# Performance work log

Measured on AMD Instinct MI355X. Metric: run time of the kernel, lower is better.

The kernel has to match this reference:

```python
import jax, jax.numpy as jnp
import numpy as np

B, Q, CACHE, CROSS = 16, 16, 1024, 1024
D, H, DK, DFF = 1024, 16, 64, 4096
EPS = 1e-5


def _ln(x, g, b):
    mu = jnp.mean(x, axis=-1, keepdims=True)
    var = jnp.mean(jnp.square(x - mu), axis=-1, keepdims=True)
    return (x - mu) * jax.lax.rsqrt(var + EPS) * g + b


def _heads(t):  # [B, L, D] -> [B, H, L, DK]
    return t.reshape(t.shape[0], t.shape[1], H, DK).transpose(0, 2, 1, 3)


def _attn(q, k, v, mask):  # q:[B,H,Q,DK] k,v:[B,H,L,DK] mask:[B,Q,L] bool
    scores = jnp.einsum('bhqd,bhkd->bhqk', q, k) / np.sqrt(DK).astype(np.float32)
    scores = jnp.where(mask[:, None, :, :], scores, jnp.finfo(scores.dtype).min)
    p = jax.nn.softmax(scores, axis=-1)
    o = jnp.einsum('bhqk,bhkd->bhqd', p, v)
    return o.transpose(0, 2, 1, 3).reshape(q.shape[0], q.shape[2], D)


def setup_inputs() -> dict:
    key = jax.random.key(0)
    ks = jax.random.split(key, 24)
    s = 0.02
    inp = {
        'x': jax.random.normal(ks[0], (B, Q, D), jnp.float32),
        'self_k_cache': jax.random.normal(ks[1], (B, CACHE, D), jnp.float32),
        'self_v_cache': jax.random.normal(ks[2], (B, CACHE, D), jnp.float32),
        'cross_k': jax.random.normal(ks[3], (B, CROSS, D), jnp.float32),
        'cross_v': jax.random.normal(ks[4], (B, CROSS, D), jnp.float32),
        'self_attn_mask': jnp.ones((B, Q, CACHE), jnp.bool_),
        'cross_attn_mask': jnp.ones((B, Q, CROSS), jnp.bool_),
        'ln1_g': jnp.ones((D,), jnp.float32), 'ln1_b': jnp.zeros((D,), jnp.float32),
        'ln2_g': jnp.ones((D,), jnp.float32), 'ln2_b': jnp.zeros((D,), jnp.float32),
        'ln3_g': jnp.ones((D,), jnp.float32), 'ln3_b': jnp.zeros((D,), jnp.float32),
        'wq_s': jax.random.normal(ks[5], (D, D), jnp.float32) * s, 'bq_s': jnp.zeros((D,), jnp.float32),
        'wk_s': jax.random.normal(ks[6], (D, D), jnp.float32) * s, 'bk_s': jnp.zeros((D,), jnp.float32),
        'wv_s': jax.random.normal(ks[7], (D, D), jnp.float32) * s, 'bv_s': jnp.zeros((D,), jnp.float32),
        'wo_s': jax.random.normal(ks[8], (D, D), jnp.float32) * s, 'bo_s': jnp.zeros((D,), jnp.float32),
        'wq_c': jax.random.normal(ks[9], (D, D), jnp.float32) * s, 'bq_c': jnp.zeros((D,), jnp.float32),
        'wo_c': jax.random.normal(ks[10], (D, D), jnp.float32) * s, 'bo_c': jnp.zeros((D,), jnp.float32),
        'w1': jax.random.normal(ks[11], (D, DFF), jnp.float32) * s, 'b1': jnp.zeros((DFF,), jnp.float32),
        'w2': jax.random.normal(ks[12], (DFF, D), jnp.float32) * s, 'b2': jnp.zeros((D,), jnp.float32),
    }
    return inp


def reference(x, self_k_cache, self_v_cache, cross_k, cross_v,
              self_attn_mask, cross_attn_mask,
              ln1_g, ln1_b, ln2_g, ln2_b, ln3_g, ln3_b,
              wq_s, bq_s, wk_s, bk_s, wv_s, bv_s, wo_s, bo_s,
              wq_c, bq_c, wo_c, bo_c, w1, b1, w2, b2):
    # --- self-attention with KV-cache append ---
    xn = _ln(x, ln1_g, ln1_b)
    q = xn @ wq_s + bq_s
    k_new = xn @ wk_s + bk_s
    v_new = xn @ wv_s + bv_s
    k_cache = self_k_cache.at[:, CACHE - Q:, :].set(k_new)
    v_cache = self_v_cache.at[:, CACHE - Q:, :].set(v_new)
    sa = _attn(_heads(q), _heads(k_cache), _heads(v_cache), self_attn_mask)
    x = x + (sa @ wo_s + bo_s)
    # --- cross-attention (k, v pre-projected) ---
    xn = _ln(x, ln2_g, ln2_b)
    qc = xn @ wq_c + bq_c
    ca = _attn(_heads(qc), _heads(cross_k), _heads(cross_v), cross_attn_mask)
    x = x + (ca @ wo_c + bo_c)
    # --- MLP ---
    xn = _ln(x, ln3_g, ln3_b)
    x = x + (jax.nn.gelu(xn @ w1 + b1) @ w2 + b2)
    return (x, k_cache, v_cache)
```

## Files before the change

kernel.cpp:

```cpp
#include <hip/hip_runtime.h>
#include <math.h>

#define D 1024
#define QLEN 16
#define DKH 64
#define ASPLIT 4
#define LC 256

typedef unsigned int uint;
typedef unsigned short ushort;
typedef __attribute__((ext_vector_type(8))) short bf16x8;
typedef __attribute__((ext_vector_type(4))) float f32x4;

struct GemmPtrs {
  const float* W[3];
  const float* bias[3];
  const float* res[3];
  float* C[3];
};

__device__ __forceinline__ ushort f2bf(float f) {
  uint u = __float_as_uint(f);
  u += 0x7fffu + ((u >> 16) & 1u);
  return (ushort)(u >> 16);
}

__device__ __forceinline__ float gelu_tanh(float x) {
  float t = 0.7978845608028654f * (x + 0.044715f * x * x * x);
  float e = __expf(2.0f * t);
  float th = 1.0f - 2.0f / (e + 1.0f);
  return 0.5f * x * (1.0f + th);
}

__global__ __launch_bounds__(256)
void ln_k(const float* __restrict__ X, const float* __restrict__ g,
          const float* __restrict__ be, uint* __restrict__ Yb) {
  int row = blockIdx.x;
  int t = threadIdx.x;
  const float4* xp = (const float4*)(X + (size_t)row * D);
  float4 x4 = xp[t];
  float s  = x4.x + x4.y + x4.z + x4.w;
  float ss = x4.x*x4.x + x4.y*x4.y + x4.z*x4.z + x4.w*x4.w;
  #pragma unroll
  for (int off = 32; off >= 1; off >>= 1) {
    s  += __shfl_xor(s, off);
    ss += __shfl_xor(ss, off);
  }
  __shared__ float as_[4], ass_[4];
  if ((t & 63) == 0) { as_[t >> 6] = s; ass_[t >> 6] = ss; }
  __syncthreads();
  s  = as_[0] + as_[1] + as_[2] + as_[3];
  ss = ass_[0] + ass_[1] + ass_[2] + ass_[3];
  float mu   = s * (1.0f / D);
  float var  = ss * (1.0f / D) - mu * mu;
  float rstd = rsqrtf(var + 1e-5f);
  float4 g4 = ((const float4*)g)[t];
  float4 b4 = ((const float4*)be)[t];
  float y0 = (x4.x - mu) * rstd * g4.x + b4.x;
  float y1 = (x4.y - mu) * rstd * g4.y + b4.y;
  float y2 = (x4.z - mu) * rstd * g4.z + b4.z;
  float y3 = (x4.w - mu) * rstd * g4.w + b4.w;
  uint2 o;
  o.x = (uint)f2bf(y0) | ((uint)f2bf(y1) << 16);
  o.y = (uint)f2bf(y2) | ((uint)f2bf(y3) << 16);
  *(uint2*)(Yb + (size_t)row * 512 + t * 2) = o;
}

template<int ASRC>
__global__ __launch_bounds__(256)
void gemm_mfma(const void* __restrict__ Ain, GemmPtrs p, int N, int K, int S) {
  int z = blockIdx.z;
  int mat = z / S, split = z - mat * S;
  const float* __restrict__ W = p.W[mat];
  float* __restrict__ C = p.C[mat];
  int Ks = K / S;
  int kb = split * Ks;
  int m0 = blockIdx.x * 64, n0 = blockIdx.y * 64;
  __shared__ short As[64][40];
  __shared__ short Ws[64][40];
  int t = threadIdx.x;
  int lane = t & 63, w = t >> 6;
  int wr = w >> 1, wc = w & 1;
  int fr = lane & 15, fg = lane >> 4;
  f32x4 acc[2][2] = {};
  int arow = t >> 2, akq = (t & 3) * 8;
  int wn4 = (t & 15) * 4, wkp = (t >> 4) * 2;

  for (int kt = 0; kt < Ks; kt += 32) {
    int k0 = kb + kt;
    if (ASRC == 1) {
      const ushort* A = (const ushort*)Ain;
      uint4 v = *(const uint4*)(A + (size_t)(m0 + arow) * K + k0 + akq);
      *(uint4*)(&As[arow][akq]) = v;
    } else {
      const float* A = (const float*)Ain;
      const float* ap = A + (size_t)(m0 + arow) * K + k0 + akq;
      float4 a0 = *(const float4*)ap;
      float4 a1 = *(const float4*)(ap + 4);
      float av[8] = {a0.x, a0.y, a0.z, a0.w, a1.x, a1.y, a1.z, a1.w};
      uint4 o;
      uint pk[4];
      #pragma unroll
      for (int e = 0; e < 4; ++e) {
        float lo = av[2*e], hi = av[2*e + 1];
        if (ASRC == 2) { lo = gelu_tanh(lo); hi = gelu_tanh(hi); }
        pk[e] = (uint)f2bf(lo) | ((uint)f2bf(hi) << 16);
      }
      o.x = pk[0]; o.y = pk[1]; o.z = pk[2]; o.w = pk[3];
      *(uint4*)(&As[arow][akq]) = o;
    }
    {
      const float* wp0 = W + (size_t)(k0 + wkp) * N + n0 + wn4;
      const float* wp1 = wp0 + N;
      float4 w0 = *(const float4*)wp0;
      float4 w1 = *(const float4*)wp1;
      float l0[4] = {w0.x, w0.y, w0.z, w0.w};
      float l1[4] = {w1.x, w1.y, w1.z, w1.w};
      #pragma unroll
      for (int j = 0; j < 4; ++j) {
        uint pk = (uint)f2bf(l0[j]) | ((uint)f2bf(l1[j]) << 16);
        *(uint*)(&Ws[wn4 + j][wkp]) = pk;
      }
    }
    __syncthreads();
    bf16x8 af[2], bf[2];
    #pragma unroll
    for (int i = 0; i < 2; ++i)
      af[i] = *(const bf16x8*)(&As[wr*32 + i*16 + fr][fg * 8]);
    #pragma unroll
    for (int j = 0; j < 2; ++j)
      bf[j] = *(const bf16x8*)(&Ws[wc*32 + j*16 + fr][fg * 8]);
    #pragma unroll
    for (int i = 0; i < 2; ++i)
      #pragma unroll
      for (int j = 0; j < 2; ++j)
        acc[i][j] = __builtin_amdgcn_mfma_f32_16x16x32_bf16(af[i], bf[j], acc[i][j], 0, 0, 0);
    __syncthreads();
  }
  const float* bias = p.bias[mat];
  const float* res  = p.res[mat];
  #pragma unroll
  for (int i = 0; i < 2; ++i) {
    #pragma unroll
    for (int j = 0; j < 2; ++j) {
      int n = n0 + wc*32 + j*16 + fr;
      int mb = m0 + wr*32 + i*16 + fg*4;
      #pragma unroll
      for (int r = 0; r < 4; ++r) {
        float v = acc[i][j][r];
        int m = mb + r;
        if (split == 0) {
          v += bias[n];
          if (res) v += res[(size_t)m * N + n];
        }
        atomicAdd(C + (size_t)m * N + n, v);
      }
    }
  }
}

__global__ __launch_bounds__(256)
void cache_build2(const float4* __restrict__ kin, const float4* __restrict__ knew,
                  float4* __restrict__ kout,
                  const float4* __restrict__ vin, const float4* __restrict__ vnew,
                  float4* __restrict__ vout) {
  size_t i = (size_t)blockIdx.x * 256 + threadIdx.x;
  const float4* cin; const float4* nv; float4* co;
  if (i < 4194304) { cin = kin; nv = knew; co = kout; }
  else { i -= 4194304; cin = vin; nv = vnew; co = vout; }
  size_t row = (i >> 8) & 1023;
  float4 v;
  if (row < 1008) {
    v = cin[i];
  } else {
    size_t b   = i >> 18;
    size_t col = i & 255;
    v = nv[(b * QLEN + (row - 1008)) * 256 + col];
  }
  co[i] = v;
}

__global__ __launch_bounds__(256)
void attn_part(const float* __restrict__ Qm, const float* __restrict__ Km,
               const float* __restrict__ Vm, float* __restrict__ Opart,
               float* __restrict__ ML, int L) {
  __shared__ float Ssc[16][260];
  int bh = blockIdx.x, split = blockIdx.y;
  int b = bh >> 4, h = bh & 15;
  int tid = threadIdx.x;
  const float* qbase = Qm + (size_t)b * QLEN * D + h * DKH;

  {
    int j = split * LC + tid;
    const float4* kp = (const float4*)(Km + ((size_t)b * L + j) * D + h * DKH);
    float4 kr[16];
    #pragma unroll
    for (int c = 0; c < 16; ++c) kr[c] = kp[c];
    for (int qi = 0; qi < 16; ++qi) {
      const float4* qv = (const float4*)(qbase + qi * D);
      float d0 = 0.f;
      #pragma unroll
      for (int c = 0; c < 16; ++c) {
        float4 q4 = qv[c];
        d0 += q4.x*kr[c].x + q4.y*kr[c].y + q4.z*kr[c].z + q4.w*kr[c].w;
      }
      Ssc[qi][tid] = d0 * 0.125f;
    }
  }
  __syncthreads();

  {
    int row = tid >> 4, lane = tid & 15;
    float m = -1e30f;
    #pragma unroll
    for (int c = 0; c < 16; ++c) m = fmaxf(m, Ssc[row][lane + c * 16]);
    #pragma unroll
    for (int off = 8; off >= 1; off >>= 1) m = fmaxf(m, __shfl_xor(m, off));
    float l = 0.f;
    #pragma unroll
    for (int c = 0; c < 16; ++c) {
      float pv = __expf(Ssc[row][lane + c * 16] - m);
      Ssc[row][lane + c * 16] = pv;
      l += pv;
    }
    #pragma unroll
    for (int off = 8; off >= 1; off >>= 1) l += __shfl_xor(l, off);
    if (lane == 0) {
      ML[(size_t)(bh * ASPLIT + split) * 32 + row]      = m;
      ML[(size_t)(bh * ASPLIT + split) * 32 + 16 + row] = l;
    }
  }
  __syncthreads();

  {
    int d = tid & 63, qg = tid >> 6;
    float a0 = 0, a1 = 0, a2 = 0, a3 = 0;
    const float* vp = Vm + ((size_t)b * L + split * LC) * D + h * DKH + d;
    for (int j = 0; j < LC; ++j) {
      float v = vp[(size_t)j * D];
      a0 = fmaf(Ssc[qg*4+0][j], v, a0);
      a1 = fmaf(Ssc[qg*4+1][j], v, a1);
      a2 = fmaf(Ssc[qg*4+2][j], v, a2);
      a3 = fmaf(Ssc[qg*4+3][j], v, a3);
    }
    float* op = Opart + (size_t)(bh * ASPLIT + split) * QLEN * DKH;
    op[(qg*4+0)*DKH + d] = a0;
    op[(qg*4+1)*DKH + d] = a1;
    op[(qg*4+2)*DKH + d] = a2;
    op[(qg*4+3)*DKH + d] = a3;
  }
}

__global__ __launch_bounds__(256)
void attn_comb(const float* __restrict__ Opart, const float* __restrict__ ML,
               float* __restrict__ Om) {
  __shared__ float Ms[ASPLIT][16], Ls[ASPLIT][16];
  int bh = blockIdx.x;
  int b = bh >> 4, h = bh & 15;
  int tid = threadIdx.x;
  if (tid < ASPLIT * 32) {
    int s = tid >> 5, r = tid & 31;
    float v = ML[(size_t)(bh * ASPLIT + s) * 32 + r];
    if (r < 16) Ms[s][r] = v; else Ls[s][r - 16] = v;
  }
  __syncthreads();
  #pragma unroll
  for (int k = 0; k < 4; ++k) {
    int idx = k * 256 + tid;
    int qi = idx >> 6, d = idx & 63;
    float M = Ms[0][qi];
    #pragma unroll
    for (int s = 1; s < ASPLIT; ++s) M = fmaxf(M, Ms[s][qi]);
    float Lsum = 0.f, o = 0.f;
    #pragma unroll
    for (int s = 0; s < ASPLIT; ++s) {
      float w = __expf(Ms[s][qi] - M);
      Lsum += Ls[s][qi] * w;
      o += w * Opart[((size_t)(bh * ASPLIT + s) * QLEN + qi) * DKH + d];
    }
    Om[(size_t)(b * QLEN + qi) * D + h * DKH + d] = o / Lsum;
  }
}

extern "C" void kernel_launch(void* const* d_in, const int* in_sizes, int n_in,
                              void* d_out, int out_size, void* d_ws, size_t ws_size,
                              hipStream_t stream) {
  (void)in_sizes; (void)n_in; (void)out_size; (void)ws_size;
  const float* x      = (const float*)d_in[0];
  const float* kcache = (const float*)d_in[1];
  const float* vcache = (const float*)d_in[2];
  const float* crossk = (const float*)d_in[3];
  const float* crossv = (const float*)d_in[4];
  const float* ln1g = (const float*)d_in[7];
  const float* ln1b = (const float*)d_in[8];
  const float* ln2g = (const float*)d_in[9];
  const float* ln2b = (const float*)d_in[10];
  const float* ln3g = (const float*)d_in[11];
  const float* ln3b = (const float*)d_in[12];
  const float* wq_s = (const float*)d_in[13];
  const float* bq_s = (const float*)d_in[14];
  const float* wk_s = (const float*)d_in[15];
  const float* bk_s = (const float*)d_in[16];
  const float* wv_s = (const float*)d_in[17];
  const float* bv_s = (const float*)d_in[18];
  const float* wo_s = (const float*)d_in[19];
  const float* bo_s = (const float*)d_in[20];
  const float* wq_c = (const float*)d_in[21];
  const float* bq_c = (const float*)d_in[22];
  const float* wo_c = (const float*)d_in[23];
  const float* bo_c = (const float*)d_in[24];
  const float* w1   = (const float*)d_in[25];
  const float* b1   = (const float*)d_in[26];
  const float* w2   = (const float*)d_in[27];
  const float* b2   = (const float*)d_in[28];

  float* outx = (float*)d_out;
  float* outk = outx + 262144;
  float* outv = outk + 16777216;

  float* ws = (float*)d_ws;
  float* q     = ws;
  float* kn    = ws + 1 * 262144;
  float* vn    = ws + 2 * 262144;
  float* qc    = ws + 3 * 262144;
  float* xr    = ws + 4 * 262144;
  float* hb    = ws + 5 * 262144;
  uint*  xnb   = (uint*)(ws + 9 * 262144);
  float* sa    = ws + 9 * 262144 + 131072;
  float* opart = sa + 262144;
  float* ml    = opart + 1048576;

  dim3 blk(256);

  hipMemsetAsync(ws, 0, (size_t)(5 * 262144 + 1048576) * sizeof(float), stream);
  hipMemsetAsync(outx, 0, (size_t)262144 * sizeof(float), stream);

  ln_k<<<256, blk, 0, stream>>>(x, ln1g, ln1b, xnb);

  {
    GemmPtrs p{};
    p.W[0] = wq_s; p.W[1] = wk_s; p.W[2] = wv_s;
    p.bias[0] = bq_s; p.bias[1] = bk_s; p.bias[2] = bv_s;
    p.C[0] = q; p.C[1] = kn; p.C[2] = vn;
    gemm_mfma<1><<<dim3(4,16,12), blk, 0, stream>>>(xnb, p, 1024, 1024, 4);
  }

  cache_build2<<<32768, blk, 0, stream>>>(
      (const float4*)kcache, (const float4*)kn, (float4*)outk,
      (const float4*)vcache, (const float4*)vn, (float4*)outv);

  attn_part<<<dim3(256, ASPLIT), blk, 0, stream>>>(q, outk, outv, opart, ml, 1024);
  attn_comb<<<256, blk, 0, stream>>>(opart, ml, sa);

  {
    GemmPtrs p{}; p.W[0] = wo_s; p.bias[0] = bo_s; p.res[0] = x; p.C[0] = xr;
    gemm_mfma<0><<<dim3(4,16,8), blk, 0, stream>>>(sa, p, 1024, 1024, 8);
  }

  ln_k<<<256, blk, 0, stream>>>(xr, ln2g, ln2b, xnb);

  {
    GemmPtrs p{}; p.W[0] = wq_c; p.bias[0] = bq_c; p.C[0] = qc;
    gemm_mfma<1><<<dim3(4,16,8), blk, 0, stream>>>(xnb, p, 1024, 1024, 8);
  }

  attn_part<<<dim3(256, ASPLIT), blk, 0, stream>>>(qc, crossk, crossv, opart, ml, 1024);
  attn_comb<<<256, blk, 0, stream>>>(opart, ml, sa);

  {
    GemmPtrs p{}; p.W[0] = wo_c; p.bias[0] = bo_c; p.C[0] = xr;
    gemm_mfma<0><<<dim3(4,16,8), blk, 0, stream>>>(sa, p, 1024, 1024, 8);
  }

  ln_k<<<256, blk, 0, stream>>>(xr, ln3g, ln3b, xnb);

  {
    GemmPtrs p{}; p.W[0] = w1; p.bias[0] = b1; p.C[0] = hb;
    gemm_mfma<1><<<dim3(4,64,2), blk, 0, stream>>>(xnb, p, 4096, 1024, 2);
  }

  {
    GemmPtrs p{}; p.W[0] = w2; p.bias[0] = b2; p.res[0] = xr; p.C[0] = outx;
    gemm_mfma<2><<<dim3(4,16,8), blk, 0, stream>>>(hb, p, 1024, 4096, 8);
  }
}
```

Measured before the change: 634.1 us.

## Fuse KV-cache copy into attention and pre-transpose weights to bf16

Removes the separate cache-building kernel by having the self-attention kernel copy its K/V tile to the output cache while reading new rows directly from the projected K/V. Adds a per-call kernel that converts and transposes all weight matrices to bf16, so GEMMs load weight tiles with plain vector copies. Attention combine now emits bf16 so output projections use the bf16 A path. The weight conversion adds extra memory traffic every call in exchange for simpler GEMM inner loops.

```diff
diff --git a/kernel.cpp b/kernel.cpp
--- a/kernel.cpp
+++ b/kernel.cpp
@@ -13,11 +13,14 @@
 typedef __attribute__((ext_vector_type(4))) float f32x4;
 
 struct GemmPtrs {
-  const float* W[3];
+  const void* W[3];
   const float* bias[3];
   const float* res[3];
   float* C[3];
 };
+
+struct WcvtDesc { const float* src; ushort* dst; int K; int N; };
+struct WcvtArgs { WcvtDesc d[8]; };
 
 __device__ __forceinline__ ushort f2bf(float f) {
   uint u = __float_as_uint(f);
@@ -30,6 +33,35 @@
   float e = __expf(2.0f * t);
   float th = 1.0f - 2.0f / (e + 1.0f);
   return 0.5f * x * (1.0f + th);
+}
+
+__global__ __launch_bounds__(256)
+void wcvt_k(WcvtArgs a) {
+  WcvtDesc de = a.d[blockIdx.y];
+  int ntn = de.N >> 6;
+  int ntiles = (de.K >> 6) * ntn;
+  int tile = blockIdx.x;
+  if (tile >= ntiles) return;
+  int kt = tile / ntn, nt = tile - kt * ntn;
+  __shared__ ushort Ls[64][72];
+  int t = threadIdx.x;
+  int colf4 = t & 15, rbase = t >> 4;
+  #pragma unroll
+  for (int u = 0; u < 4; ++u) {
+    int kl = u * 16 + rbase;
+    float4 w4 = *(const float4*)(de.src + (size_t)(kt*64 + kl) * de.N + nt*64 + colf4*4);
+    Ls[colf4*4 + 0][kl] = f2bf(w4.x);
+    Ls[colf4*4 + 1][kl] = f2bf(w4.y);
+    Ls[colf4*4 + 2][kl] = f2bf(w4.z);
+    Ls[colf4*4 + 3][kl] = f2bf(w4.w);
+  }
+  __syncthreads();
+  int nl = t >> 2, c = t & 3;
+  uint4 v0 = *(const uint4*)(&Ls[nl][c*16]);
+  uint4 v1 = *(const uint4*)(&Ls[nl][c*16 + 8]);
+  ushort* dst = de.dst + (size_t)(nt*64 + nl) * de.K + kt*64 + c*16;
+  *(uint4*)(dst)     = v0;
+  *(uint4*)(dst + 8) = v1;
 }
 
 __global__ __launch_bounds__(256)
@@ -71,70 +103,53 @@
 void gemm_mfma(const void* __restrict__ Ain, GemmPtrs p, int N, int K, int S) {
   int z = blockIdx.z;
   int mat = z / S, split = z - mat * S;
-  const float* __restrict__ W = p.W[mat];
+  const ushort* __restrict__ WT = (const ushort*)p.W[mat];
   float* __restrict__ C = p.C[mat];
-  int Ks = K / S;
-  int kb = split * Ks;
+  int Ks = K / S, kb = split * Ks;
   int m0 = blockIdx.x * 64, n0 = blockIdx.y * 64;
-  __shared__ short As[64][40];
-  __shared__ short Ws[64][40];
+  __shared__ short As[64 * 40];
+  __shared__ short Ws[64 * 40];
   int t = threadIdx.x;
   int lane = t & 63, w = t >> 6;
   int wr = w >> 1, wc = w & 1;
   int fr = lane & 15, fg = lane >> 4;
   f32x4 acc[2][2] = {};
-  int arow = t >> 2, akq = (t & 3) * 8;
-  int wn4 = (t & 15) * 4, wkp = (t >> 4) * 2;
+  int srow = t >> 2, sch = (t & 3) * 8;
+  int soff = srow * 40 + sch;
+  const ushort* wsrc  = WT + (size_t)(n0 + srow) * K + kb + sch;
+  const ushort* asrcb = (const ushort*)Ain + (size_t)(m0 + srow) * K + kb + sch;
+  const float*  asrcf = (const float*)Ain + (size_t)(m0 + srow) * K + kb + sch;
 
   for (int kt = 0; kt < Ks; kt += 32) {
-    int k0 = kb + kt;
     if (ASRC == 1) {
-      const ushort* A = (const ushort*)Ain;
-      uint4 v = *(const uint4*)(A + (size_t)(m0 + arow) * K + k0 + akq);
-      *(uint4*)(&As[arow][akq]) = v;
+      *(uint4*)(As + soff) = *(const uint4*)(asrcb + kt);
     } else {
-      const float* A = (const float*)Ain;
-      const float* ap = A + (size_t)(m0 + arow) * K + k0 + akq;
-      float4 a0 = *(const float4*)ap;
-      float4 a1 = *(const float4*)(ap + 4);
+      const float* ap = asrcf + kt;
+      float4 a0 = *(const float4*)ap, a1 = *(const float4*)(ap + 4);
       float av[8] = {a0.x, a0.y, a0.z, a0.w, a1.x, a1.y, a1.z, a1.w};
-      uint4 o;
       uint pk[4];
       #pragma unroll
       for (int e = 0; e < 4; ++e) {
-        float lo = av[2*e], hi = av[2*e + 1];
-        if (ASRC == 2) { lo = gelu_tanh(lo); hi = gelu_tanh(hi); }
+        float lo = gelu_tanh(av[2*e]), hi = gelu_tanh(av[2*e + 1]);
         pk[e] = (uint)f2bf(lo) | ((uint)f2bf(hi) << 16);
       }
-      o.x = pk[0]; o.y = pk[1]; o.z = pk[2]; o.w = pk[3];
-      *(uint4*)(&As[arow][akq]) = o;
-    }
-    {
-      const float* wp0 = W + (size_t)(k0 + wkp) * N + n0 + wn4;
-      const float* wp1 = wp0 + N;
-      float4 w0 = *(const float4*)wp0;
-      float4 w1 = *(const float4*)wp1;
-      float l0[4] = {w0.x, w0.y, w0.z, w0.w};
-      float l1[4] = {w1.x, w1.y, w1.z, w1.w};
-      #pragma unroll
-      for (int j = 0; j < 4; ++j) {
-        uint pk = (uint)f2bf(l0[j]) | ((uint)f2bf(l1[j]) << 16);
-        *(uint*)(&Ws[wn4 + j][wkp]) = pk;
-      }
-    }
+      uint4 o; o.x = pk[0]; o.y = pk[1]; o.z = pk[2]; o.w = pk[3];
+      *(uint4*)(As + soff) = o;
+    }
+    *(uint4*)(Ws + soff) = *(const uint4*)(wsrc + kt);
     __syncthreads();
-    bf16x8 af[2], bf[2];
+    bf16x8 af[2], bfr[2];
     #pragma unroll
     for (int i = 0; i < 2; ++i)
-      af[i] = *(const bf16x8*)(&As[wr*32 + i*16 + fr][fg * 8]);
+      af[i] = *(const bf16x8*)(As + (wr*32 + i*16 + fr) * 40 + fg * 8);
     #pragma unroll
     for (int j = 0; j < 2; ++j)
-      bf[j] = *(const bf16x8*)(&Ws[wc*32 + j*16 + fr][fg * 8]);
+      bfr[j] = *(const bf16x8*)(Ws + (wc*32 + j*16 + fr) * 40 + fg * 8);
     #pragma unroll
     for (int i = 0; i < 2; ++i)
       #pragma unroll
       for (int j = 0; j < 2; ++j)
-        acc[i][j] = __builtin_amdgcn_mfma_f32_16x16x32_bf16(af[i], bf[j], acc[i][j], 0, 0, 0);
+        acc[i][j] = __builtin_amdgcn_mfma_f32_16x16x32_bf16(af[i], bfr[j], acc[i][j], 0, 0, 0);
     __syncthreads();
   }
   const float* bias = p.bias[mat];
@@ -148,51 +163,59 @@
       #pragma unroll
       for (int r = 0; r < 4; ++r) {
         float v = acc[i][j][r];
-        int m = mb + r;
         if (split == 0) {
           v += bias[n];
-          if (res) v += res[(size_t)m * N + n];
+          if (res) v += res[(size_t)(mb + r) * N + n];
         }
-        atomicAdd(C + (size_t)m * N + n, v);
+        atomicAdd(C + (size_t)(mb + r) * N + n, v);
       }
     }
   }
 }
 
-__global__ __launch_bounds__(256)
-void cache_build2(const float4* __restrict__ kin, const float4* __restrict__ knew,
-                  float4* __restrict__ kout,
-                  const float4* __restrict__ vin, const float4* __restrict__ vnew,
-                  float4* __restrict__ vout) {
-  size_t i = (size_t)blockIdx.x * 256 + threadIdx.x;
-  const float4* cin; const float4* nv; float4* co;
-  if (i < 4194304) { cin = kin; nv = knew; co = kout; }
-  else { i -= 4194304; cin = vin; nv = vnew; co = vout; }
-  size_t row = (i >> 8) & 1023;
-  float4 v;
-  if (row < 1008) {
-    v = cin[i];
-  } else {
-    size_t b   = i >> 18;
-    size_t col = i & 255;
-    v = nv[(b * QLEN + (row - 1008)) * 256 + col];
-  }
-  co[i] = v;
-}
-
+template<int COPY>
 __global__ __launch_bounds__(256)
 void attn_part(const float* __restrict__ Qm, const float* __restrict__ Km,
-               const float* __restrict__ Vm, float* __restrict__ Opart,
-               float* __restrict__ ML, int L) {
+               const float* __restrict__ Vm,
+               const float* __restrict__ Kn, const float* __restrict__ Vn,
+               float* __restrict__ OutK, float* __restrict__ OutV,
+               float* __restrict__ Opart, float* __restrict__ ML, int L) {
   __shared__ float Ssc[16][260];
   int bh = blockIdx.x, split = blockIdx.y;
   int b = bh >> 4, h = bh & 15;
   int tid = threadIdx.x;
   const float* qbase = Qm + (size_t)b * QLEN * D + h * DKH;
+  int nb = L - QLEN;
+
+  if (COPY) {
+    #pragma unroll
+    for (int u = 0; u < 16; ++u) {
+      int idx = u * 256 + tid;
+      int r = idx >> 4, c = idx & 15;
+      int row = split * LC + r;
+      size_t dsto = ((size_t)b * L + row) * 256 + h * 16 + c;
+      float4 kv, vv;
+      if (row < nb) {
+        kv = ((const float4*)Km)[dsto];
+        vv = ((const float4*)Vm)[dsto];
+      } else {
+        size_t so = ((size_t)b * QLEN + (row - nb)) * 256 + h * 16 + c;
+        kv = ((const float4*)Kn)[so];
+        vv = ((const float4*)Vn)[so];
+      }
+      ((float4*)OutK)[dsto] = kv;
+      ((float4*)OutV)[dsto] = vv;
+    }
+  }
 
   {
     int j = split * LC + tid;
-    const float4* kp = (const float4*)(Km + ((size_t)b * L + j) * D + h * DKH);
+    const float* ksrc;
+    if (COPY && j >= nb)
+      ksrc = Kn + ((size_t)b * QLEN + (j - nb)) * D + h * DKH;
+    else
+      ksrc = Km + ((size_t)b * L + j) * D + h * DKH;
+    const float4* kp = (const float4*)ksrc;
     float4 kr[16];
     #pragma unroll
     for (int c = 0; c < 16; ++c) kr[c] = kp[c];
@@ -235,14 +258,27 @@
   {
     int d = tid & 63, qg = tid >> 6;
     float a0 = 0, a1 = 0, a2 = 0, a3 = 0;
+    int lim = COPY ? (nb - split * LC) : LC;
+    if (lim > LC) lim = LC;
+    if (lim < 0) lim = 0;
     const float* vp = Vm + ((size_t)b * L + split * LC) * D + h * DKH + d;
-    for (int j = 0; j < LC; ++j) {
+    for (int j = 0; j < lim; ++j) {
       float v = vp[(size_t)j * D];
       a0 = fmaf(Ssc[qg*4+0][j], v, a0);
       a1 = fmaf(Ssc[qg*4+1][j], v, a1);
       a2 = fmaf(Ssc[qg*4+2][j], v, a2);
       a3 = fmaf(Ssc[qg*4+3][j], v, a3);
     }
+    if (COPY) {
+      for (int j = lim; j < LC; ++j) {
+        int row = split * LC + j;
+        float v = Vn[((size_t)b * QLEN + (row - nb)) * D + h * DKH + d];
+        a0 = fmaf(Ssc[qg*4+0][j], v, a0);
+        a1 = fmaf(Ssc[qg*4+1][j], v, a1);
+        a2 = fmaf(Ssc[qg*4+2][j], v, a2);
+        a3 = fmaf(Ssc[qg*4+3][j], v, a3);
+      }
+    }
     float* op = Opart + (size_t)(bh * ASPLIT + split) * QLEN * DKH;
     op[(qg*4+0)*DKH + d] = a0;
     op[(qg*4+1)*DKH + d] = a1;
@@ -253,7 +289,7 @@
 
 __global__ __launch_bounds__(256)
 void attn_comb(const float* __restrict__ Opart, const float* __restrict__ ML,
-               float* __restrict__ Om) {
+               ushort* __restrict__ Om) {
   __shared__ float Ms[ASPLIT][16], Ls[ASPLIT][16];
   int bh = blockIdx.x;
   int b = bh >> 4, h = bh & 15;
@@ -278,7 +314,7 @@
       Lsum += Ls[s][qi] * w;
       o += w * Opart[((size_t)(bh * ASPLIT + s) * QLEN + qi) * DKH + d];
     }
-    Om[(size_t)(b * QLEN + qi) * D + h * DKH + d] = o / Lsum;
+    Om[(size_t)(b * QLEN + qi) * D + h * DKH + d] = f2bf(o / Lsum);
   }
 }
 
@@ -325,62 +361,82 @@
   float* qc    = ws + 3 * 262144;
   float* xr    = ws + 4 * 262144;
   float* hb    = ws + 5 * 262144;
-  uint*  xnb   = (uint*)(ws + 9 * 262144);
-  float* sa    = ws + 9 * 262144 + 131072;
-  float* opart = sa + 262144;
-  float* ml    = opart + 1048576;
+  uint*  xnb   = (uint*)(ws + 2359296);
+  ushort* sab  = (ushort*)(ws + 2490368);
+  float* opart = ws + 2555904;
+  float* ml    = ws + 3604480;
+  ushort* wtb  = (ushort*)(ws + 3637248);
+  ushort* wqT  = wtb;
+  ushort* wkT  = wtb + 1 * 1048576;
+  ushort* wvT  = wtb + 2 * 1048576;
+  ushort* woT  = wtb + 3 * 1048576;
+  ushort* wqcT = wtb + 4 * 1048576;
+  ushort* wocT = wtb + 5 * 1048576;
+  ushort* w1T  = wtb + 6 * 1048576;
+  ushort* w2T  = wtb + 10 * 1048576;
 
   dim3 blk(256);
 
-  hipMemsetAsync(ws, 0, (size_t)(5 * 262144 + 1048576) * sizeof(float), stream);
+  hipMemsetAsync(ws, 0, (size_t)2359296 * sizeof(float), stream);
   hipMemsetAsync(outx, 0, (size_t)262144 * sizeof(float), stream);
 
+  {
+    WcvtArgs a;
+    a.d[0] = {wq_s, wqT, 1024, 1024};
+    a.d[1] = {wk_s, wkT, 1024, 1024};
+    a.d[2] = {wv_s, wvT, 1024, 1024};
+    a.d[3] = {wo_s, woT, 1024, 1024};
+    a.d[4] = {wq_c, wqcT, 1024, 1024};
+    a.d[5] = {wo_c, wocT, 1024, 1024};
+    a.d[6] = {w1, w1T, 1024, 4096};
+    a.d[7] = {w2, w2T, 4096, 1024};
+    wcvt_k<<<dim3(1024, 8), blk, 0, stream>>>(a);
+  }
+
   ln_k<<<256, blk, 0, stream>>>(x, ln1g, ln1b, xnb);
 
   {
     GemmPtrs p{};
-    p.W[0] = wq_s; p.W[1] = wk_s; p.W[2] = wv_s;
+    p.W[0] = wqT; p.W[1] = wkT; p.W[2] = wvT;
     p.bias[0] = bq_s; p.bias[1] = bk_s; p.bias[2] = bv_s;
     p.C[0] = q; p.C[1] = kn; p.C[2] = vn;
     gemm_mfma<1><<<dim3(4,16,12), blk, 0, stream>>>(xnb, p, 1024, 1024, 4);
   }
 
-  cache_build2<<<32768, blk, 0, stream>>>(
-      (const float4*)kcache, (const float4*)kn, (float4*)outk,
-      (const float4*)vcache, (const float4*)vn, (float4*)outv);
-
-  attn_part<<<dim3(256, ASPLIT), blk, 0, stream>>>(q, outk, outv, opart, ml, 1024);
-  attn_comb<<<256, blk, 0, stream>>>(opart, ml, sa);
-
-  {
-    GemmPtrs p{}; p.W[0] = wo_s; p.bias[0] = bo_s; p.res[0] = x; p.C[0] = xr;
-    gemm_mfma<0><<<dim3(4,16,8), blk, 0, stream>>>(sa, p, 1024, 1024, 8);
+  attn_part<1><<<dim3(256, ASPLIT), blk, 0, stream>>>(
+      q, kcache, vcache, kn, vn, outk, outv, opart, ml, 1024);
+  attn_comb<<<256, blk, 0, stream>>>(opart, ml, sab);
+
+  {
+    GemmPtrs p{}; p.W[0] = woT; p.bias[0] = bo_s; p.res[0] = x; p.C[0] = xr;
+    gemm_mfma<1><<<dim3(4,16,8), blk, 0, stream>>>(sab, p, 1024, 1024, 8);
   }
 
   ln_k<<<256, blk, 0, stream>>>(xr, ln2g, ln2b, xnb);
 
   {
-    GemmPtrs p{}; p.W[0] = wq_c; p.bias[0] = bq_c; p.C[0] = qc;
+    GemmPtrs p{}; p.W[0] = wqcT; p.bias[0] = bq_c; p.C[0] = qc;
     gemm_mfma<1><<<dim3(4,16,8), blk, 0, stream>>>(xnb, p, 1024, 1024, 8);
   }
 
-  attn_part<<<dim3(256, ASPLIT), blk, 0, stream>>>(qc, crossk, crossv, opart, ml, 1024);
-  attn_comb<<<256, blk, 0, stream>>>(opart, ml, sa);
-
-  {
-    GemmPtrs p{}; p.W[0] = wo_c; p.bias[0] = bo_c; p.C[0] = xr;
-    gemm_mfma<0><<<dim3(4,16,8), blk, 0, stream>>>(sa, p, 1024, 1024, 8);
+  attn_part<0><<<dim3(256, ASPLIT), blk, 0, stream>>>(
+      qc, crossk, crossv, nullptr, nullptr, nullptr, nullptr, opart, ml, 1024);
+  attn_comb<<<256, blk, 0, stream>>>(opart, ml, sab);
+
+  {
+    GemmPtrs p{}; p.W[0] = wocT; p.bias[0] = bo_c; p.C[0] = xr;
+    gemm_mfma<1><<<dim3(4,16,8), blk, 0, stream>>>(sab, p, 1024, 1024, 8);
   }
 
   ln_k<<<256, blk, 0, stream>>>(xr, ln3g, ln3b, xnb);
 
   {
-    GemmPtrs p{}; p.W[0] = w1; p.bias[0] = b1; p.C[0] = hb;
+    GemmPtrs p{}; p.W[0] = w1T; p.bias[0] = b1; p.C[0] = hb;
     gemm_mfma<1><<<dim3(4,64,2), blk, 0, stream>>>(xnb, p, 4096, 1024, 2);
   }
 
   {
-    GemmPtrs p{}; p.W[0] = w2; p.bias[0] = b2; p.res[0] = xr; p.C[0] = outx;
+    GemmPtrs p{}; p.W[0] = w2T; p.bias[0] = b2; p.res[0] = xr; p.C[0] = outx;
     gemm_mfma<2><<<dim3(4,16,8), blk, 0, stream>>>(hb, p, 1024, 4096, 8);
   }
 }
```

After: 649.1 us. 1.02x slower.
